# Kernel optimization log

Measured on AMD Instinct MI355X. Metric: run time of the kernel, lower is better.

The kernel has to match this reference:

```python
import jax, jax.numpy as jnp
import numpy as np

B, S, R, D, A, P = 64, 128, 8, 10000, 10, 256


def setup_inputs() -> dict:
    key = jax.random.key(0)
    ks = jax.random.split(key, 7)
    return {
        "atom_hvs": jax.random.normal(ks[0], (A, D), jnp.float32),
        "pos_hvs": jax.random.normal(ks[1], (S, D), jnp.float32),
        "closure_tag": jax.random.normal(ks[2], (D,), jnp.float32),
        "W": jax.random.normal(ks[3], (P, D), jnp.float32) / np.float32(np.sqrt(D)),
        "b": jax.random.normal(ks[4], (P,), jnp.float32) * 0.01,
        "token_mask": jnp.ones((B, S), jnp.float32),
        "ring_mask": jnp.ones((B, R), jnp.float32),
        "atom_idx": jax.random.randint(ks[5], (B, S), 0, A),
        "ring_pos": jax.random.randint(ks[6], (B, R, 2), 0, S),
    }


def reference(atom_hvs, pos_hvs, closure_tag, W, b, token_mask, ring_mask, atom_idx, ring_pos):
    # HRR bind = circular convolution -> pointwise multiply in rFFT domain.
    # Bundle = sum; by linearity we sum in the frequency domain and do a
    # single irfft per molecule (same math as per-token conv + add).
    d = atom_hvs.shape[-1]
    Fa = jnp.fft.rfft(atom_hvs, axis=-1)          # [A, F]
    Fp = jnp.fft.rfft(pos_hvs, axis=-1)           # [S, F]
    Fc = jnp.fft.rfft(closure_tag)                # [F]

    s = atom_idx.shape[1]
    tok = Fa[atom_idx] * Fp[None, :s, :]          # [B, S, F] gather+bind
    freq = jnp.sum(token_mask[..., None] * tok, axis=1)   # [B, F] bundle

    ring = Fp[ring_pos[..., 0]] * Fp[ring_pos[..., 1]] * Fc  # [B, R, F]
    freq = freq + jnp.sum(ring_mask[..., None] * ring, axis=1)

    mol_hv = jnp.fft.irfft(freq, n=d, axis=-1)    # [B, D]
    return mol_hv @ W.T + b                       # [B, proj_dim]
```

## Files before the change

### kernel.cpp

```cpp
#include <hip/hip_runtime.h>

#define PI2 6.28318530717958647692f

#define NSIG 139
#define FS   5120

__global__ __launch_bounds__(256) void k_fwd(
                     const float* __restrict__ atom, const float* __restrict__ pos,
                     const float* __restrict__ clo, float2* __restrict__ spec) {
  __shared__ float xs[5000];
  unsigned sig = blockIdx.x, q = blockIdx.y;
  unsigned k1base = q * 10u;
  unsigned nk1 = (k1base + 10u <= 51u) ? 10u : (51u - k1base);
  const float* xb = (sig < 128u) ? (pos + sig * 10000u)
                   : ((sig < 138u) ? (atom + (sig - 128u) * 10000u) : clo);
  int tid = threadIdx.x;
  unsigned ntile1 = nk1 * 25u;
  unsigned k1l = tid / 25u, n2 = (tid % 25u) * 4u;
  bool have = (unsigned)tid < ntile1;
  unsigned k1 = k1base + k1l;
  float cth, sth;
  __sincosf(PI2 * (float)k1 * 0.01f, &sth, &cth);
  float c = 1.0f, s = 0.0f;
  float ar[4] = {}, as[4] = {};

  for (int h = 0; h < 2; ++h) {
    for (int i = tid; i < 1250; i += 256)
      *(float4*)(xs + 4 * i) = *(const float4*)(xb + h * 5000 + 4 * i);
    __syncthreads();
    if (have) {
#pragma unroll 5
      for (int n1l = 0; n1l < 50; ++n1l) {
        const float4 xv = *(const float4*)(xs + n1l * 100 + n2);
        ar[0] += xv.x * c; as[0] += xv.x * s;
        ar[1] += xv.y * c; as[1] += xv.y * s;
        ar[2] += xv.z * c; as[2] += xv.z * s;
        ar[3] += xv.w * c; as[3] += xv.w * s;
        float cn = c * cth - s * sth;
        float sn = s * cth + c * sth;
        c = cn; s = sn;
      }
    }
    __syncthreads();
  }

  if (have) {
    unsigned rb = (100u - k1) % 100u;
    float resA[8], resB[8];
#pragma unroll
    for (int j = 0; j < 4; ++j) {
      float swA, cwA, swB, cwB;
      __sincosf(PI2 * (float)((n2 + j) * k1) * 1e-4f, &swA, &cwA);
      __sincosf(PI2 * (float)((n2 + j) * rb) * 1e-4f, &swB, &cwB);
      resA[2 * j + 0] = ar[j] * cwA - as[j] * swA;
      resA[2 * j + 1] = -(as[j] * cwA + ar[j] * swA);
      resB[2 * j + 0] = ar[j] * cwB + as[j] * swB;
      resB[2 * j + 1] = as[j] * cwB - ar[j] * swB;
    }
    float* pA = xs + k1l * 200u + n2 * 2u;
    float* pB = xs + (nk1 + k1l) * 200u + n2 * 2u;
    *(float4*)(pA + 0) = make_float4(resA[0], resA[1], resA[2], resA[3]);
    *(float4*)(pA + 4) = make_float4(resA[4], resA[5], resA[6], resA[7]);
    *(float4*)(pB + 0) = make_float4(resB[0], resB[1], resB[2], resB[3]);
    *(float4*)(pB + 4) = make_float4(resB[4], resB[5], resB[6], resB[7]);
  }
  __syncthreads();

  unsigned nrow = 2u * nk1;
  unsigned ntile3 = nrow * 26u;
  for (unsigned t = tid; t < ntile3; t += 256u) {
    unsigned lr = t / 26u, k2 = (t % 26u) * 2u;
    unsigned gk1 = (lr < nk1) ? (k1base + lr) : ((100u - (k1base + (lr - nk1))) % 100u);
    const float* brow = xs + lr * 200u;
    float cthA, sthA, cthB, sthB;
    __sincosf(PI2 * (float)k2 * 0.01f, &sthA, &cthA);
    __sincosf(PI2 * (float)(k2 + 1) * 0.01f, &sthB, &cthB);
    float cA = 1.0f, sA = 0.0f, cB = 1.0f, sB = 0.0f;
    float reA = 0.f, imA = 0.f, reB = 0.f, imB = 0.f;
#pragma unroll 4
    for (int n2i = 0; n2i < 100; n2i += 2) {
      const float4 b0 = *(const float4*)(brow + 2 * n2i);
      reA += b0.x * cA + b0.y * sA;  imA += b0.y * cA - b0.x * sA;
      reB += b0.x * cB + b0.y * sB;  imB += b0.y * cB - b0.x * sB;
      float cA1 = cA * cthA - sA * sthA, sA1 = sA * cthA + cA * sthA;
      float cB1 = cB * cthB - sB * sthB, sB1 = sB * cthB + cB * sthB;
      reA += b0.z * cA1 + b0.w * sA1;  imA += b0.w * cA1 - b0.z * sA1;
      reB += b0.z * cB1 + b0.w * sB1;  imB += b0.w * cB1 - b0.z * sB1;
      cA = cA1 * cthA - sA1 * sthA; sA = sA1 * cthA + cA1 * sthA;
      cB = cB1 * cthB - sB1 * sthB; sB = sB1 * cthB + cB1 * sthB;
    }
    unsigned kA = gk1 + 100u * k2;
    unsigned kB = gk1 + 100u * (k2 + 1);
    if (kA <= 5000u) spec[sig * FS + kA] = make_float2(reA, imA);
    if (kB <= 5000u) spec[sig * FS + kB] = make_float2(reB, imB);
  }
}

__global__ void k_mix(const float2* __restrict__ spec,
                      const float* __restrict__ tmask, const float* __restrict__ rmask,
                      const int* __restrict__ aidx, const int* __restrict__ rpos,
                      float2* __restrict__ G) {
  __shared__ float2 FaS[10][256];
  __shared__ float2 FcS[256];
  __shared__ float tmS[2][128];
  __shared__ int   aiS[2][128];
  __shared__ float rmS[2][8];
  __shared__ int   rpS[2][8][2];
  int tid = threadIdx.x;
  int k = blockIdx.x * 256 + tid;
  int kc = k > 5000 ? 5000 : k;
  int b0 = blockIdx.y * 2;
#pragma unroll
  for (int a = 0; a < 10; ++a) FaS[a][tid] = spec[(128 + a) * FS + kc];
  FcS[tid] = spec[138 * FS + kc];
  for (int i = tid; i < 2 * 128; i += 256) {
    int bb = i >> 7, ss = i & 127;
    tmS[bb][ss] = tmask[(b0 + bb) * 128 + ss];
    aiS[bb][ss] = aidx[(b0 + bb) * 128 + ss];
  }
  if (tid < 16) {
    int bb = tid >> 3, rr = tid & 7;
    rmS[bb][rr] = rmask[(b0 + bb) * 8 + rr];
    rpS[bb][rr][0] = rpos[((b0 + bb) * 8 + rr) * 2 + 0];
    rpS[bb][rr][1] = rpos[((b0 + bb) * 8 + rr) * 2 + 1];
  }
  __syncthreads();
  float fr[2] = {}, fi[2] = {};
#pragma unroll 8
  for (int s = 0; s < 128; ++s) {
    float2 fp = spec[s * FS + kc];
#pragma unroll
    for (int b = 0; b < 2; ++b) {
      int a = aiS[b][s];
      float tm = tmS[b][s];
      float2 fa = FaS[a][tid];
      float tr = fa.x * fp.x - fa.y * fp.y;
      float ti = fa.x * fp.y + fa.y * fp.x;
      fr[b] += tm * tr;
      fi[b] += tm * ti;
    }
  }
  float2 fc = FcS[tid];
#pragma unroll
  for (int r = 0; r < 8; ++r) {
#pragma unroll
    for (int b = 0; b < 2; ++b) {
      int p0 = rpS[b][r][0], p1 = rpS[b][r][1];
      float rm = rmS[b][r];
      float2 f0 = spec[p0 * FS + kc];
      float2 f1 = spec[p1 * FS + kc];
      float tr = f0.x * f1.x - f0.y * f1.y;
      float ti = f0.x * f1.y + f0.y * f1.x;
      float ur = tr * fc.x - ti * fc.y;
      float ui = tr * fc.y + ti * fc.x;
      fr[b] += rm * ur;
      fi[b] += rm * ui;
    }
  }
  if (k <= 5000) {
#pragma unroll
    for (int b = 0; b < 2; ++b) {
      float fib = (k == 0 || k == 5000) ? 0.0f : fi[b];
      G[(size_t)(b0 + b) * 10000 + k] = make_float2(fr[b], fib);
      if (k >= 1 && k <= 4999)
        G[(size_t)(b0 + b) * 10000 + (10000 - k)] = make_float2(fr[b], -fib);
    }
  }
}

__global__ void k_i1(const float2* __restrict__ G, float2* __restrict__ Bi) {
  __shared__ float gs[10400];
  unsigned sig = blockIdx.x;
  const float* gp = (const float*)(G + sig * 10000u);
  for (int i = threadIdx.x; i < 2600; i += 256) {
    int row = i / 26, c4 = i % 26;
    *(float4*)(gs + row * 104 + c4 * 4) = *(const float4*)(gp + row * 200 + c4 * 4);
  }
  __syncthreads();
  unsigned tt = blockIdx.y * 256u + threadIdx.x;
  if (tt >= 1300u) return;
  unsigned m1 = (tt / 26u) * 2u, n2 = (tt % 26u) * 2u;
  float cthA, sthA, cthB, sthB;
  __sincosf(PI2 * (float)m1 * 0.01f, &sthA, &cthA);
  __sincosf(PI2 * (float)(m1 + 1) * 0.01f, &sthB, &cthB);
  float cA = 1.0f, sA = 0.0f, cB = 1.0f, sB = 0.0f;
  float reA[2] = {}, imA[2] = {};
  float reB[2] = {}, imB[2] = {};
#pragma unroll 4
  for (int n1 = 0; n1 < 100; ++n1) {
    const float4 gv = *(const float4*)(gs + n1 * 104 + n2 * 2);
    reA[0] += gv.x * cA - gv.y * sA;  imA[0] += gv.y * cA + gv.x * sA;
    reB[0] += gv.z * cA - gv.w * sA;  imB[0] += gv.w * cA + gv.z * sA;
    reA[1] += gv.x * cB - gv.y * sB;  imA[1] += gv.y * cB + gv.x * sB;
    reB[1] += gv.z * cB - gv.w * sB;  imB[1] += gv.w * cB + gv.z * sB;
    float cA1 = cA * cthA - sA * sthA, sA1 = sA * cthA + cA * sthA;
    float cB1 = cB * cthB - sB * sthB, sB1 = sB * cthB + cB * sthB;
    cA = cA1; sA = sA1; cB = cB1; sB = sB1;
  }
  float w0 = (n2 == 0 || n2 == 50) ? 0.5f : 1.0f;
  float w1 = (n2 == 50) ? 0.0f : 1.0f;
#pragma unroll
  for (int i = 0; i < 2; ++i) {
    float sw0, cw0, sw1, cw1;
    __sincosf(PI2 * (float)(n2 * (m1 + i)) * 1e-4f, &sw0, &cw0);
    __sincosf(PI2 * (float)((n2 + 1) * (m1 + i)) * 1e-4f, &sw1, &cw1);
    float4 outv;
    outv.x = (reA[i] * cw0 - imA[i] * sw0) * w0;
    outv.y = (imA[i] * cw0 + reA[i] * sw0) * w0;
    outv.z = (reB[i] * cw1 - imB[i] * sw1) * w1;
    outv.w = (imB[i] * cw1 + reB[i] * sw1) * w1;
    *(float4*)((float*)Bi + (sig * 5200u + (m1 + i) * 52u + n2) * 2) = outv;
  }
}

__global__ void k_i2(const float2* __restrict__ Bi, float* __restrict__ mol) {
  __shared__ float bs[10400];
  unsigned sig = blockIdx.x;
  const float* bp = (const float*)Bi + sig * 10400u;
  for (int i = threadIdx.x; i < 2600; i += 256)
    *(float4*)(bs + 4 * i) = *(const float4*)(bp + 4 * i);
  __syncthreads();
  unsigned tt = blockIdx.y * 256u + threadIdx.x;
  if (tt >= 2500u) return;
  unsigned m1 = (tt / 50u) * 2u;
  unsigned m2 = (tt % 50u) * 2u;
  const float* b0 = bs + m1 * 104u;
  const float* b1 = b0 + 104;
  float cthA, sthA, cthB, sthB;
  __sincosf(PI2 * (float)m2 * 0.01f, &sthA, &cthA);
  __sincosf(PI2 * (float)(m2 + 1) * 0.01f, &sthB, &cthB);
  float cA = 1.0f, sA = 0.0f, cB = 1.0f, sB = 0.0f;
  float re[2][2] = {};
#pragma unroll 4
  for (int jj = 0; jj < 26; ++jj) {
    int n2 = 2 * jj;
    const float4 v0 = *(const float4*)(b0 + 2 * n2);
    const float4 v1 = *(const float4*)(b1 + 2 * n2);
    re[0][0] += v0.x * cA - v0.y * sA;
    re[1][0] += v1.x * cA - v1.y * sA;
    re[0][1] += v0.x * cB - v0.y * sB;
    re[1][1] += v1.x * cB - v1.y * sB;
    float cA1 = cA * cthA - sA * sthA, sA1 = sA * cthA + cA * sthA;
    float cB1 = cB * cthB - sB * sthB, sB1 = sB * cthB + cB * sthB;
    re[0][0] += v0.z * cA1 - v0.w * sA1;
    re[1][0] += v1.z * cA1 - v1.w * sA1;
    re[0][1] += v0.z * cB1 - v0.w * sB1;
    re[1][1] += v1.z * cB1 - v1.w * sB1;
    cA = cA1 * cthA - sA1 * sthA; sA = sA1 * cthA + cA1 * sthA;
    cB = cB1 * cthB - sB1 * sthB; sB = sB1 * cthB + cB1 * sthB;
  }
#pragma unroll
  for (int i = 0; i < 2; ++i)
#pragma unroll
    for (int j = 0; j < 2; ++j)
      mol[sig * 10000u + (m1 + i) + 100u * (m2 + j)] = re[i][j] * 2e-4f;
}

__global__ __launch_bounds__(256) void k_proj(const float* __restrict__ mol,
                                              const float* __restrict__ W,
                                              float* __restrict__ part) {
  __shared__ float molS[40 * 64];
  int tid = threadIdx.x;
  int d0 = blockIdx.x * 40;
  for (int i = tid; i < 40 * 64; i += 256)
    molS[i] = mol[(size_t)(i & 63) * 10000 + d0 + (i >> 6)];
  __syncthreads();
  int p0 = (tid & 63) * 4;
  int bh = (tid >> 6) * 16;
  float acc[4][16] = {};
  const float* w0 = W + (size_t)(p0 + 0) * 10000 + d0;
  const float* w1 = W + (size_t)(p0 + 1) * 10000 + d0;
  const float* w2 = W + (size_t)(p0 + 2) * 10000 + d0;
  const float* w3 = W + (size_t)(p0 + 3) * 10000 + d0;
#pragma unroll 4
  for (int dl = 0; dl < 40; ++dl) {
    const float wv[4] = {w0[dl], w1[dl], w2[dl], w3[dl]};
    const float4* m4 = (const float4*)(molS + dl * 64 + bh);
#pragma unroll
    for (int q = 0; q < 4; ++q) {
      float4 mv = m4[q];
#pragma unroll
      for (int pp = 0; pp < 4; ++pp) {
        acc[pp][4 * q + 0] += wv[pp] * mv.x;
        acc[pp][4 * q + 1] += wv[pp] * mv.y;
        acc[pp][4 * q + 2] += wv[pp] * mv.z;
        acc[pp][4 * q + 3] += wv[pp] * mv.w;
      }
    }
  }
#pragma unroll
  for (int b = 0; b < 16; ++b) {
    float4 v = make_float4(acc[0][b], acc[1][b], acc[2][b], acc[3][b]);
    *(float4*)(part + (size_t)blockIdx.x * 16384 + (bh + b) * 256 + p0) = v;
  }
}

__global__ void k_red(const float* __restrict__ part, const float* __restrict__ bias,
                      float* __restrict__ out) {
  int tid = threadIdx.x;
  int b = blockIdx.x;
  float acc = bias[tid];
#pragma unroll 8
  for (int ch = 0; ch < 250; ++ch)
    acc += part[(size_t)ch * 16384 + b * 256 + tid];
  out[b * 256 + tid] = acc;
}

extern "C" void kernel_launch(void* const* d_in, const int* in_sizes, int n_in,
                              void* d_out, int out_size, void* d_ws, size_t ws_size,
                              hipStream_t stream) {
  const float* atom  = (const float*)d_in[0];
  const float* pos   = (const float*)d_in[1];
  const float* clo   = (const float*)d_in[2];
  const float* W     = (const float*)d_in[3];
  const float* bias  = (const float*)d_in[4];
  const float* tmask = (const float*)d_in[5];
  const float* rmask = (const float*)d_in[6];
  const int*   aidx  = (const int*)d_in[7];
  const int*   rpos  = (const int*)d_in[8];
  float* out = (float*)d_out;

  char* ws = (char*)d_ws;
  size_t off = 0;
  auto alloc = [&](size_t n) { off = (off + 255) & ~(size_t)255; size_t o = off; off += n; return o; };
  char* regA   = ws + alloc(16777216);
  float2* Bi   = (float2*)regA;
  float*  part = (float*)regA;
  float2* spec = (float2*)(ws + alloc((size_t)NSIG * FS * 8));
  float2* G    = (float2*)(ws + alloc((size_t)64 * 10000 * 8));
  float*  mol  = (float*)(ws + alloc((size_t)64 * 10000 * 4));

  k_fwd<<<dim3(NSIG, 6), dim3(256), 0, stream>>>(atom, pos, clo, spec);
  k_mix<<<dim3(20, 32), dim3(256), 0, stream>>>(spec, tmask, rmask, aidx, rpos, G);
  k_i1<<<dim3(64, 6), dim3(256), 0, stream>>>(G, Bi);
  k_i2<<<dim3(64, 10), dim3(256), 0, stream>>>(Bi, mol);
  k_proj<<<dim3(250), dim3(256), 0, stream>>>(mol, W, part);
  k_red<<<dim3(64), dim3(256), 0, stream>>>(part, bias, out);
}
```

Measured before the change: 191.0 us.

## Fuse two inverse DFT stages into one kernel with shared-memory intermediate

Merges the two inverse-DFT passes into a single kernel. Each block handles ten output rows of one signal. It streams the frequency data through shared memory in two halves, writes the twiddled intermediate to shared memory, and then runs the second pass from there. This removes the global round trip of the intermediate buffer and one kernel launch. In exchange, each block reloads the full signal's spectrum, so global reads of G grow roughly tenfold across the grid, and block occupancy is lower.

```diff
diff --git a/kernel.cpp b/kernel.cpp
--- a/kernel.cpp
+++ b/kernel.cpp
@@ -168,92 +168,95 @@
   }
 }
 
-__global__ void k_i1(const float2* __restrict__ G, float2* __restrict__ Bi) {
-  __shared__ float gs[10400];
-  unsigned sig = blockIdx.x;
+__global__ __launch_bounds__(256) void k_inv(const float2* __restrict__ G,
+                                             float* __restrict__ mol) {
+  __shared__ float gs[5200];
+  __shared__ float biS[1040];
+  unsigned sig = blockIdx.x, md = blockIdx.y;
+  unsigned m1base = md * 10u;
+  int tid = threadIdx.x;
   const float* gp = (const float*)(G + sig * 10000u);
-  for (int i = threadIdx.x; i < 2600; i += 256) {
-    int row = i / 26, c4 = i % 26;
-    *(float4*)(gs + row * 104 + c4 * 4) = *(const float4*)(gp + row * 200 + c4 * 4);
+
+  float reA[2] = {}, imA[2] = {}, reB[2] = {}, imB[2] = {};
+
+  for (int h = 0; h < 2; ++h) {
+    if (h) __syncthreads();
+    for (int i = tid; i < 1300; i += 256) {
+      int row = i / 26, c4 = i % 26;
+      *(float4*)(gs + row * 104 + c4 * 4) =
+          *(const float4*)(gp + (h * 50 + row) * 200 + c4 * 4);
+    }
+    __syncthreads();
+#pragma unroll
+    for (int r = 0; r < 2; ++r) {
+      unsigned t = (unsigned)tid + 256u * r;
+      if (t >= 260u) continue;
+      unsigned m1l = t / 26u, n2 = (t % 26u) * 2u;
+      unsigned m1 = m1base + m1l;
+      float cth, sth;
+      __sincosf(PI2 * (float)m1 * 0.01f, &sth, &cth);
+      float c, s;
+      if (h == 0) { c = 1.0f; s = 0.0f; }
+      else        { c = (m1 & 1u) ? -1.0f : 1.0f; s = 0.0f; }
+      float ra = reA[r], ia = imA[r], rb = reB[r], ib = imB[r];
+#pragma unroll 5
+      for (int n1l = 0; n1l < 50; ++n1l) {
+        const float4 gv = *(const float4*)(gs + n1l * 104 + n2 * 2);
+        ra += gv.x * c - gv.y * s;  ia += gv.y * c + gv.x * s;
+        rb += gv.z * c - gv.w * s;  ib += gv.w * c + gv.z * s;
+        float cn = c * cth - s * sth;
+        float sn = s * cth + c * sth;
+        c = cn; s = sn;
+      }
+      reA[r] = ra; imA[r] = ia; reB[r] = rb; imB[r] = ib;
+    }
+  }
+#pragma unroll
+  for (int r = 0; r < 2; ++r) {
+    unsigned t = (unsigned)tid + 256u * r;
+    if (t >= 260u) continue;
+    unsigned m1l = t / 26u, n2 = (t % 26u) * 2u;
+    unsigned m1 = m1base + m1l;
+    float w0 = (n2 == 0u || n2 == 50u) ? 0.5f : 1.0f;
+    float w1 = (n2 == 50u) ? 0.0f : 1.0f;
+    float sw0, cw0, sw1, cw1;
+    __sincosf(PI2 * (float)(n2 * m1) * 1e-4f, &sw0, &cw0);
+    __sincosf(PI2 * (float)((n2 + 1u) * m1) * 1e-4f, &sw1, &cw1);
+    float4 outv;
+    outv.x = (reA[r] * cw0 - imA[r] * sw0) * w0;
+    outv.y = (imA[r] * cw0 + reA[r] * sw0) * w0;
+    outv.z = (reB[r] * cw1 - imB[r] * sw1) * w1;
+    outv.w = (imB[r] * cw1 + reB[r] * sw1) * w1;
+    *(float4*)(biS + m1l * 104u + n2 * 2u) = outv;
   }
   __syncthreads();
-  unsigned tt = blockIdx.y * 256u + threadIdx.x;
-  if (tt >= 1300u) return;
-  unsigned m1 = (tt / 26u) * 2u, n2 = (tt % 26u) * 2u;
-  float cthA, sthA, cthB, sthB;
-  __sincosf(PI2 * (float)m1 * 0.01f, &sthA, &cthA);
-  __sincosf(PI2 * (float)(m1 + 1) * 0.01f, &sthB, &cthB);
-  float cA = 1.0f, sA = 0.0f, cB = 1.0f, sB = 0.0f;
-  float reA[2] = {}, imA[2] = {};
-  float reB[2] = {}, imB[2] = {};
+
+  for (int t = tid; t < 500; t += 256) {
+    unsigned l = (unsigned)t / 50u;
+    unsigned m2 = ((unsigned)t % 50u) * 2u;
+    const float* b0 = biS + l * 104u;
+    float cthA, sthA, cthB, sthB;
+    __sincosf(PI2 * (float)m2 * 0.01f, &sthA, &cthA);
+    __sincosf(PI2 * (float)(m2 + 1u) * 0.01f, &sthB, &cthB);
+    float cA = 1.0f, sA = 0.0f, cB = 1.0f, sB = 0.0f;
+    float r0 = 0.f, r1 = 0.f;
 #pragma unroll 4
-  for (int n1 = 0; n1 < 100; ++n1) {
-    const float4 gv = *(const float4*)(gs + n1 * 104 + n2 * 2);
-    reA[0] += gv.x * cA - gv.y * sA;  imA[0] += gv.y * cA + gv.x * sA;
-    reB[0] += gv.z * cA - gv.w * sA;  imB[0] += gv.w * cA + gv.z * sA;
-    reA[1] += gv.x * cB - gv.y * sB;  imA[1] += gv.y * cB + gv.x * sB;
-    reB[1] += gv.z * cB - gv.w * sB;  imB[1] += gv.w * cB + gv.z * sB;
-    float cA1 = cA * cthA - sA * sthA, sA1 = sA * cthA + cA * sthA;
-    float cB1 = cB * cthB - sB * sthB, sB1 = sB * cthB + cB * sthB;
-    cA = cA1; sA = sA1; cB = cB1; sB = sB1;
-  }
-  float w0 = (n2 == 0 || n2 == 50) ? 0.5f : 1.0f;
-  float w1 = (n2 == 50) ? 0.0f : 1.0f;
-#pragma unroll
-  for (int i = 0; i < 2; ++i) {
-    float sw0, cw0, sw1, cw1;
-    __sincosf(PI2 * (float)(n2 * (m1 + i)) * 1e-4f, &sw0, &cw0);
-    __sincosf(PI2 * (float)((n2 + 1) * (m1 + i)) * 1e-4f, &sw1, &cw1);
-    float4 outv;
-    outv.x = (reA[i] * cw0 - imA[i] * sw0) * w0;
-    outv.y = (imA[i] * cw0 + reA[i] * sw0) * w0;
-    outv.z = (reB[i] * cw1 - imB[i] * sw1) * w1;
-    outv.w = (imB[i] * cw1 + reB[i] * sw1) * w1;
-    *(float4*)((float*)Bi + (sig * 5200u + (m1 + i) * 52u + n2) * 2) = outv;
-  }
-}
-
-__global__ void k_i2(const float2* __restrict__ Bi, float* __restrict__ mol) {
-  __shared__ float bs[10400];
-  unsigned sig = blockIdx.x;
-  const float* bp = (const float*)Bi + sig * 10400u;
-  for (int i = threadIdx.x; i < 2600; i += 256)
-    *(float4*)(bs + 4 * i) = *(const float4*)(bp + 4 * i);
-  __syncthreads();
-  unsigned tt = blockIdx.y * 256u + threadIdx.x;
-  if (tt >= 2500u) return;
-  unsigned m1 = (tt / 50u) * 2u;
-  unsigned m2 = (tt % 50u) * 2u;
-  const float* b0 = bs + m1 * 104u;
-  const float* b1 = b0 + 104;
-  float cthA, sthA, cthB, sthB;
-  __sincosf(PI2 * (float)m2 * 0.01f, &sthA, &cthA);
-  __sincosf(PI2 * (float)(m2 + 1) * 0.01f, &sthB, &cthB);
-  float cA = 1.0f, sA = 0.0f, cB = 1.0f, sB = 0.0f;
-  float re[2][2] = {};
-#pragma unroll 4
-  for (int jj = 0; jj < 26; ++jj) {
-    int n2 = 2 * jj;
-    const float4 v0 = *(const float4*)(b0 + 2 * n2);
-    const float4 v1 = *(const float4*)(b1 + 2 * n2);
-    re[0][0] += v0.x * cA - v0.y * sA;
-    re[1][0] += v1.x * cA - v1.y * sA;
-    re[0][1] += v0.x * cB - v0.y * sB;
-    re[1][1] += v1.x * cB - v1.y * sB;
-    float cA1 = cA * cthA - sA * sthA, sA1 = sA * cthA + cA * sthA;
-    float cB1 = cB * cthB - sB * sthB, sB1 = sB * cthB + cB * sthB;
-    re[0][0] += v0.z * cA1 - v0.w * sA1;
-    re[1][0] += v1.z * cA1 - v1.w * sA1;
-    re[0][1] += v0.z * cB1 - v0.w * sB1;
-    re[1][1] += v1.z * cB1 - v1.w * sB1;
-    cA = cA1 * cthA - sA1 * sthA; sA = sA1 * cthA + cA1 * sthA;
-    cB = cB1 * cthB - sB1 * sthB; sB = sB1 * cthB + cB1 * sthB;
-  }
-#pragma unroll
-  for (int i = 0; i < 2; ++i)
-#pragma unroll
-    for (int j = 0; j < 2; ++j)
-      mol[sig * 10000u + (m1 + i) + 100u * (m2 + j)] = re[i][j] * 2e-4f;
+    for (int jj = 0; jj < 26; ++jj) {
+      int n2i = 2 * jj;
+      const float4 v0 = *(const float4*)(b0 + 2 * n2i);
+      r0 += v0.x * cA - v0.y * sA;
+      r1 += v0.x * cB - v0.y * sB;
+      float cA1 = cA * cthA - sA * sthA, sA1 = sA * cthA + cA * sthA;
+      float cB1 = cB * cthB - sB * sthB, sB1 = sB * cthB + cB * sthB;
+      r0 += v0.z * cA1 - v0.w * sA1;
+      r1 += v0.z * cB1 - v0.w * sB1;
+      cA = cA1 * cthA - sA1 * sthA; sA = sA1 * cthA + cA1 * sthA;
+      cB = cB1 * cthB - sB1 * sthB; sB = sB1 * cthB + cB1 * sthB;
+    }
+    unsigned m1g = m1base + l;
+    mol[sig * 10000u + m1g + 100u * m2] = r0 * 2e-4f;
+    mol[sig * 10000u + m1g + 100u * (m2 + 1u)] = r1 * 2e-4f;
+  }
 }
 
 __global__ __launch_bounds__(256) void k_proj(const float* __restrict__ mol,
@@ -323,17 +326,14 @@
   char* ws = (char*)d_ws;
   size_t off = 0;
   auto alloc = [&](size_t n) { off = (off + 255) & ~(size_t)255; size_t o = off; off += n; return o; };
-  char* regA   = ws + alloc(16777216);
-  float2* Bi   = (float2*)regA;
-  float*  part = (float*)regA;
+  float*  part = (float*)(ws + alloc(16777216));
   float2* spec = (float2*)(ws + alloc((size_t)NSIG * FS * 8));
   float2* G    = (float2*)(ws + alloc((size_t)64 * 10000 * 8));
   float*  mol  = (float*)(ws + alloc((size_t)64 * 10000 * 4));
 
   k_fwd<<<dim3(NSIG, 6), dim3(256), 0, stream>>>(atom, pos, clo, spec);
   k_mix<<<dim3(20, 32), dim3(256), 0, stream>>>(spec, tmask, rmask, aidx, rpos, G);
-  k_i1<<<dim3(64, 6), dim3(256), 0, stream>>>(G, Bi);
-  k_i2<<<dim3(64, 10), dim3(256), 0, stream>>>(Bi, mol);
+  k_inv<<<dim3(64, 10), dim3(256), 0, stream>>>(G, mol);
   k_proj<<<dim3(250), dim3(256), 0, stream>>>(mol, W, part);
   k_red<<<dim3(64), dim3(256), 0, stream>>>(part, bias, out);
 }
```

After: 195.2 us. 1.02x slower.
